# Kernel tuning notes

Hardware: AMD Instinct MI355X
Metric: run time of the kernel (lower is better)

Reference implementation:

```python
import jax, jax.numpy as jnp
import numpy as np

HIDDEN = 3072
HEADS = 32
HEAD_DIM = HIDDEN // HEADS  # 96


def setup_inputs() -> dict:
    key = jax.random.key(0)
    k1, k2, k3, k4 = jax.random.split(key, 4)
    B, S = 2, 2048
    x = jax.random.normal(k1, (B, S, HIDDEN), dtype=jnp.float32)
    # qkv_proj: Linear(hidden, 3*hidden, bias=False); torch weight is [out,in]
    w_qkv = jax.random.normal(k2, (3 * HIDDEN, HIDDEN), dtype=jnp.float32) * (HIDDEN ** -0.5)
    # o_proj: Linear(hidden, hidden) with bias
    w_o = jax.random.normal(k3, (HIDDEN, HIDDEN), dtype=jnp.float32) * (HIDDEN ** -0.5)
    b_o = jax.random.normal(k4, (HIDDEN,), dtype=jnp.float32) * 0.01
    return {"x": x, "w_qkv": w_qkv, "w_o": w_o, "b_o": b_o}


def reference(x, w_qkv, w_o, b_o):
    B, S, _ = x.shape
    qkv = jnp.einsum('bsh,oh->bso', x, w_qkv)  # [B,S,3*HIDDEN]
    q, k, v = jnp.split(qkv, 3, axis=-1)
    # [B,S,HIDDEN] -> [B,H,S,D]
    def split_heads(t):
        return t.reshape(B, S, HEADS, HEAD_DIM).transpose(0, 2, 1, 3)
    q, k, v = split_heads(q), split_heads(k), split_heads(v)
    scores = jnp.einsum('bhqd,bhkd->bhqk', q, k) / jnp.sqrt(jnp.float32(HEAD_DIM))
    attn = jax.nn.softmax(scores, axis=-1)
    out = jnp.einsum('bhqk,bhkd->bhqd', attn, v)  # [B,H,S,D]
    out = out.transpose(0, 2, 1, 3).reshape(B, S, HIDDEN)
    return jnp.einsum('bsh,oh->bso', out, w_o) + b_o
```

## Files before the change

### kernel.cpp

```cpp
#include <hip/hip_runtime.h>
#include <math.h>


typedef unsigned int u32;
typedef unsigned short u16;
typedef __attribute__((ext_vector_type(8))) short bf16x8;
typedef __attribute__((ext_vector_type(4))) float f32x4;
typedef __attribute__((ext_vector_type(16))) float f32x16;

#define MFMA(a, b, c) __builtin_amdgcn_mfma_f32_16x16x32_bf16((a), (b), (c), 0, 0, 0)
#define MFMA32(a, b, c) __builtin_amdgcn_mfma_f32_32x32x16_bf16((a), (b), (c), 0, 0, 0)

#define GLDS16(g, l) __builtin_amdgcn_global_load_lds( \
    (const __attribute__((address_space(1))) u32*)(g), \
    (__attribute__((address_space(3))) u32*)(l), 16, 0, 0)

__device__ __forceinline__ u16 f2bf(float f) {
  u32 u = __builtin_bit_cast(u32, f);
  return (u16)((u + 0x7fffu + ((u >> 16) & 1u)) >> 16);
}
__device__ __forceinline__ float bf2f(u16 h) {
  u32 u = ((u32)h) << 16;
  return __builtin_bit_cast(float, u);
}
__device__ __forceinline__ void split2(float f, u16& h, u16& l) {
  h = f2bf(f);
  l = f2bf(f - bf2f(h));
}
__device__ __forceinline__ bf16x8 ld16(const u16* p) {
  return *reinterpret_cast<const bf16x8*>(p);
}

__global__ void split_kernel(const float* __restrict__ src, u16* __restrict__ dst,
                             long n) {
  long i = ((long)blockIdx.x * 256 + threadIdx.x) * 4;
  if (i >= n) return;
  const float4 v = *reinterpret_cast<const float4*>(src + i);
  const u32 i32 = (u32)i;
  const u32 row = i32 / 3072u;
  const u32 col = i32 - row * 3072u;
  const long base = (long)row * 6144 + (col >> 5) * 64 + (col & 31);
  ushort4 h, l;
  split2(v.x, h.x, l.x);
  split2(v.y, h.y, l.y);
  split2(v.z, h.z, l.z);
  split2(v.w, h.w, l.w);
  *reinterpret_cast<ushort4*>(dst + base) = h;
  *reinterpret_cast<ushort4*>(dst + base + 32) = l;
}

template <int MODE>
__global__ __launch_bounds__(256, 2) void gemm32(
    const u16* __restrict__ A2, const u16* __restrict__ B2,
    int M, int N,
    u16* __restrict__ C2, float* __restrict__ Cf, const float* __restrict__ bias) {
  constexpr int NT = 96;
  __shared__ u16 ldsA[2][128 * 64];
  __shared__ u16 ldsB[2][192 * 64];
  const int tid = threadIdx.x;
  const int lane = tid & 63;
  const int w = tid >> 6;
  const int wm = w >> 1, wn = w & 1;
  const int l31 = lane & 31;
  const int l5 = lane >> 5;

  const int mt = M >> 7;
  const int nwg = gridDim.x;
  const int bid = blockIdx.x;
  const int wg = (bid & 7) * (nwg >> 3) + (bid >> 3);
  const int bm = wg % mt, bn = wg / mt;

  const int srow = lane >> 3;
  const int sgc = ((lane & 7) ^ srow ^ w) * 8;

  auto stA = [&](int buf, int kt, int j) {
    const int r = j * 32 + w * 8 + srow;
    GLDS16(A2 + (long)(bm * 128 + r) * 6144 + kt * 64 + sgc,
           &ldsA[buf][(j * 32 + w * 8) * 64]);
  };
  auto stB = [&](int buf, int kt, int j) {
    const int r = j * 32 + w * 8 + srow;
    GLDS16(B2 + (long)(bn * 192 + r) * 6144 + kt * 64 + sgc,
           &ldsB[buf][(j * 32 + w * 8) * 64]);
  };

  f32x16 acc[2][3];
#pragma unroll
  for (int m = 0; m < 2; ++m)
#pragma unroll
    for (int n = 0; n < 3; ++n)
#pragma unroll
      for (int j = 0; j < 16; ++j) acc[m][n][j] = 0.f;

  stA(0, 0, 0); stA(0, 0, 1); stA(0, 0, 2); stA(0, 0, 3);
  stB(0, 0, 0); stB(0, 0, 1); stB(0, 0, 2);
  stB(0, 0, 3); stB(0, 0, 4); stB(0, 0, 5);
  __syncthreads();

  const int aRow0 = wm * 64 + l31;
  const int bRow0 = wn * 96 + l31;
  const int rk = (lane & 7) ^ ((lane >> 3) & 3);

#define CSLOT(KS, PL) ((((KS)*2 + l5 + (PL)*4) ^ rk) * 8)
#define RD_PH(KS)                                                          \
  _Pragma("unroll") for (int n = 0; n < 3; ++n) {                          \
    const int off = (bRow0 + n * 32) * 64;                                 \
    b[n][0] = ld16(&LB[off + CSLOT(KS, 0)]);                               \
    b[n][1] = ld16(&LB[off + CSLOT(KS, 1)]);                               \
  }                                                                        \
  _Pragma("unroll") for (int m = 0; m < 2; ++m) {                          \
    const int off = (aRow0 + m * 32) * 64;                                 \
    a[m][0] = ld16(&LA[off + CSLOT(KS, 0)]);                               \
    a[m][1] = ld16(&LA[off + CSLOT(KS, 1)]);                               \
  }
#define DO_MFMA3()                                                         \
  __builtin_amdgcn_s_setprio(1);                                           \
  _Pragma("unroll") for (int m = 0; m < 2; ++m)                            \
  _Pragma("unroll") for (int n = 0; n < 3; ++n) {                          \
    acc[m][n] = MFMA32(a[m][0], b[n][0], acc[m][n]);                       \
    acc[m][n] = MFMA32(a[m][0], b[n][1], acc[m][n]);                       \
    acc[m][n] = MFMA32(a[m][1], b[n][0], acc[m][n]);                       \
  }                                                                        \
  __builtin_amdgcn_s_setprio(0);
#define PH_SYNC()                                                          \
  __builtin_amdgcn_s_barrier();                                            \
  asm volatile("s_waitcnt lgkmcnt(0)" ::: "memory");                       \
  __builtin_amdgcn_sched_barrier(0);

  for (int t = 0; t < NT; ++t) {
    const int cur = t & 1;
    const int nxt = cur ^ 1;
    const u16* LA = ldsA[cur];
    const u16* LB = ldsB[cur];
    bf16x8 a[2][2], b[3][2];
    RD_PH(0);
    if (t + 1 < NT) {
      stA(nxt, t + 1, 0); stA(nxt, t + 1, 1);
      stA(nxt, t + 1, 2); stA(nxt, t + 1, 3);
      stB(nxt, t + 1, 0); stB(nxt, t + 1, 1); stB(nxt, t + 1, 2);
      stB(nxt, t + 1, 3); stB(nxt, t + 1, 4); stB(nxt, t + 1, 5);
    }
    PH_SYNC();
    DO_MFMA3();
    __builtin_amdgcn_s_barrier();
    RD_PH(1);
    PH_SYNC();
    DO_MFMA3();
    asm volatile("s_waitcnt vmcnt(0)" ::: "memory");
    __builtin_amdgcn_s_barrier();
  }
#undef CSLOT
#undef RD_PH
#undef DO_MFMA3
#undef PH_SYNC

#pragma unroll
  for (int mf = 0; mf < 2; ++mf)
#pragma unroll
    for (int nf = 0; nf < 3; ++nf) {
      const int col = bn * 192 + wn * 96 + nf * 32 + l31;
#pragma unroll
      for (int reg = 0; reg < 16; ++reg) {
        const int rif = (reg & 3) + 8 * (reg >> 2) + 4 * l5;
        const long row = (long)bm * 128 + wm * 64 + mf * 32 + rif;
        const float v = acc[mf][nf][reg];
        if (MODE == 0) {
          const long idx = row * (2L * N) + (col >> 5) * 64 + (col & 31);
          u16 h, l;
          split2(v, h, l);
          C2[idx] = h;
          C2[idx + 32] = l;
        } else {
          Cf[row * N + col] = v + bias[col];
        }
      }
    }
}

__global__ void pack_k(const u16* __restrict__ QKV2, u16* __restrict__ Kp) {
  const int t = blockIdx.x * 256 + threadIdx.x;
  const int lane = t & 63;
  const int rec3 = t >> 6;
  const int c = rec3 % 3;
  const int kb = (rec3 / 3) & 127;
  const int hl = rec3 / 384;
  const int lr = lane & 15, lg = lane >> 4;
  const long src = ((long)((hl >> 5) * 2048 + kb * 16 + lr)) * 18432 +
                   (96 + (hl & 31) * 3 + c) * 64 + lg * 8;
  const long dst = ((long)rec3 * 2) * 512 + lane * 8;
  *reinterpret_cast<bf16x8*>(Kp + dst) = ld16(QKV2 + src);
  *reinterpret_cast<bf16x8*>(Kp + dst + 512) = ld16(QKV2 + src + 32);
}

__global__ __launch_bounds__(256) void pack_v(const u16* __restrict__ QKV2,
                                              u16* __restrict__ Vp) {
  __shared__ u16 sV[2][32 * 96];
  const int tid = threadIdx.x;
  const int hl = blockIdx.x >> 6;
  const int kq = blockIdx.x & 63;
  const long rowbase = ((long)((hl >> 5) * 2048 + kq * 32)) * 18432 +
                       (192 + (hl & 31) * 3) * 64;
#pragma unroll
  for (int i = 0; i < 3; ++i) {
    const int idx = i * 256 + tid;
    const int pl = idx / 384;
    const int r2 = idx % 384;
    const int row = r2 / 12, cu = r2 % 12;
    const long src = rowbase + (long)row * 18432 + (cu >> 2) * 64 + (cu & 3) * 8 + pl * 32;
    *reinterpret_cast<bf16x8*>(&sV[pl][row * 96 + cu * 8]) = ld16(QKV2 + src);
  }
  __syncthreads();
#pragma unroll
  for (int i = 0; i < 3; ++i) {
    const int idx = i * 256 + tid;
    const int lane = idx & 63;
    const int rl = idx >> 6;
    const int n = rl >> 1, pl = rl & 1;
    const int lr = lane & 15, lg = lane >> 4;
    bf16x8 o;
#pragma unroll
    for (int e = 0; e < 8; ++e) o[e] = (short)sV[pl][(lg * 8 + e) * 96 + n * 16 + lr];
    const long dst = ((((long)hl * 6 + n) * 64 + kq) * 2 + pl) * 512 + lane * 8;
    *reinterpret_cast<bf16x8*>(Vp + dst) = o;
  }
}

__global__ __launch_bounds__(256, 2) void attn_kernel(
    const u16* __restrict__ QKV2,
    const u16* __restrict__ Kp, const u16* __restrict__ Vp,
    u16* __restrict__ AO2) {
  __shared__ u16 kv[2][24 * 512];
  __shared__ u16 pb[4][2][2][512];
  const int lane = threadIdx.x & 63;
  const int wv = threadIdx.x >> 6;
  const int lr = lane & 15, lg = lane >> 4;

  const int nwg = gridDim.x;
  const int bid = blockIdx.x;
  const int wg = (bid & 7) * (nwg >> 3) + (bid >> 3);
  const int hl = wg >> 4;
  const int qblk = wg & 15;
  const int b = hl >> 5;
  const int q0 = qblk * 128 + wv * 32;

  bf16x8 qh[2][3], ql[2][3];
#pragma unroll
  for (int f = 0; f < 2; ++f) {
    const long qofs =
        ((long)(b * 2048 + q0 + f * 16 + lr)) * 18432 + ((hl & 31) * 3) * 64 + lg * 8;
#pragma unroll
    for (int c = 0; c < 3; ++c) {
      qh[f][c] = ld16(QKV2 + qofs + c * 64);
      ql[f][c] = ld16(QKV2 + qofs + c * 64 + 32);
    }
  }

  f32x4 o_acc[2][6];
#pragma unroll
  for (int f = 0; f < 2; ++f)
#pragma unroll
    for (int n = 0; n < 6; ++n)
#pragma unroll
      for (int j = 0; j < 4; ++j) o_acc[f][n][j] = 0.f;
  float lsum[2][4] = {{0.f, 0.f, 0.f, 0.f}, {0.f, 0.f, 0.f, 0.f}};

  const float scale = 0.10206207261596577f;

  auto stage = [&](int nb, int it) {
    const long kbase = ((long)hl * 768 + (long)it * 12) * 512;
    const long vbase = ((long)hl * 768 + (long)it * 2) * 512;
#pragma unroll
    for (int j = 0; j < 6; ++j) {
      const int r = wv * 6 + j;
      const u16* src;
      if (r < 12) {
        const int tt = r / 6, rc = r % 6;
        src = Kp + kbase + ((long)(tt * 6 + rc)) * 512 + lane * 8;
      } else {
        const int r2 = r - 12;
        src = Vp + vbase + ((long)((r2 >> 1) * 128 + (r2 & 1))) * 512 + lane * 8;
      }
      GLDS16(src, &kv[nb][r * 512]);
    }
  };

  stage(0, 0);
  __syncthreads();

  for (int it = 0; it < 64; ++it) {
    const int nb = it & 1;
    if (it < 63) stage(nb ^ 1, it + 1);
    const u16* L = kv[nb];

    bf16x8 kh0[3], kl0[3], kh1[3], kl1[3];
#pragma unroll
    for (int c = 0; c < 3; ++c) {
      kh0[c] = ld16(L + (c * 2 + 0) * 512 + lane * 8);
      kl0[c] = ld16(L + (c * 2 + 1) * 512 + lane * 8);
      kh1[c] = ld16(L + (6 + c * 2 + 0) * 512 + lane * 8);
      kl1[c] = ld16(L + (6 + c * 2 + 1) * 512 + lane * 8);
    }

    bf16x8 pah[2], pal[2];
#pragma unroll
    for (int f = 0; f < 2; ++f) {
      f32x4 s0, s1;
#pragma unroll
      for (int j = 0; j < 4; ++j) { s0[j] = 0.f; s1[j] = 0.f; }
#pragma unroll
      for (int c = 0; c < 3; ++c) {
        s0 = MFMA(qh[f][c], kh0[c], s0);
        s1 = MFMA(qh[f][c], kh1[c], s1);
        s0 = MFMA(qh[f][c], kl0[c], s0);
        s1 = MFMA(qh[f][c], kl1[c], s1);
        s0 = MFMA(ql[f][c], kh0[c], s0);
        s1 = MFMA(ql[f][c], kh1[c], s1);
      }
      u16* pbh = pb[wv][f][0];
      u16* pbl = pb[wv][f][1];
#pragma unroll
      for (int j = 0; j < 4; ++j) {
        const float p0 = __expf(fmaf(s0[j], scale, -12.f));
        const float p1 = __expf(fmaf(s1[j], scale, -12.f));
        lsum[f][j] += p0 + p1;
        const int r = lg * 4 + j;
        const int key = j ^ lg;
        u16 h, l;
        split2(p0, h, l);
        const int a0 = r * 32 + ((((lr >> 3) ^ key) & 3) << 3) + (lr & 7);
        pbh[a0] = h;
        pbl[a0] = l;
        split2(p1, h, l);
        const int a1 = r * 32 + ((((2 + (lr >> 3)) ^ key) & 3) << 3) + (lr & 7);
        pbh[a1] = h;
        pbl[a1] = l;
      }
      const int rkey = (lr & 3) ^ (lr >> 2);
      const int ra = lr * 32 + (((lg ^ rkey) & 3) << 3);
      pah[f] = ld16(&pbh[ra]);
      pal[f] = ld16(&pbl[ra]);
    }

#pragma unroll
    for (int n = 0; n < 6; ++n) {
      const bf16x8 vh = ld16(L + (12 + n * 2 + 0) * 512 + lane * 8);
      const bf16x8 vl = ld16(L + (12 + n * 2 + 1) * 512 + lane * 8);
#pragma unroll
      for (int f = 0; f < 2; ++f) {
        o_acc[f][n] = MFMA(pah[f], vh, o_acc[f][n]);
        o_acc[f][n] = MFMA(pah[f], vl, o_acc[f][n]);
        o_acc[f][n] = MFMA(pal[f], vh, o_acc[f][n]);
      }
    }
    __syncthreads();
  }

#pragma unroll
  for (int f = 0; f < 2; ++f) {
    float inv[4];
#pragma unroll
    for (int j = 0; j < 4; ++j) {
      float rs = lsum[f][j];
#pragma unroll
      for (int mk = 1; mk < 16; mk <<= 1) rs += __shfl_xor(rs, mk);
      inv[j] = 1.f / rs;
    }
#pragma unroll
    for (int n = 0; n < 6; ++n)
#pragma unroll
      for (int j = 0; j < 4; ++j) {
        const long row = (long)(b * 2048 + q0 + f * 16 + lg * 4 + j);
        const long idx =
            row * 6144 + ((hl & 31) * 3 + (n >> 1)) * 64 + (n & 1) * 16 + lr;
        u16 h, l;
        split2(o_acc[f][n][j] * inv[j], h, l);
        AO2[idx] = h;
        AO2[idx + 32] = l;
      }
  }
}

extern "C" void kernel_launch(void* const* d_in, const int* in_sizes, int n_in,
                              void* d_out, int out_size, void* d_ws, size_t ws_size,
                              hipStream_t stream) {
  const float* x = (const float*)d_in[0];
  const float* wqkv = (const float*)d_in[1];
  const float* wo = (const float*)d_in[2];
  const float* bo = (const float*)d_in[3];
  float* out = (float*)d_out;
  char* ws = (char*)d_ws;

  const size_t E_X = (size_t)4096 * 3072;
  const size_t E_WQ = (size_t)9216 * 3072;
  const size_t E_QKV = (size_t)4096 * 9216;
  const size_t E_WO = (size_t)3072 * 3072;

  u16* X2 = (u16*)ws;
  char* W0 = ws + 4 * E_X;
  u16* W2 = (u16*)W0;
  char* Q0 = W0 + 4 * E_WQ;
  u16* QKV2 = (u16*)Q0;
  char* V0 = Q0 + 4 * E_QKV;
  u16* VP = (u16*)V0;
  u16* KP = (u16*)ws;
  u16* AO2 = (u16*)W0;
  u16* WO2 = (u16*)(W0 + 4 * E_X);

  const size_t need = 4 * (E_X + E_WQ + E_QKV + E_X);
  if (ws_size < need) return;

  split_kernel<<<12288, 256, 0, stream>>>(x, X2, (long)E_X);
  split_kernel<<<27648, 256, 0, stream>>>(wqkv, W2, (long)E_WQ);
  gemm32<0><<<1536, 256, 0, stream>>>(X2, W2, 4096, 9216, QKV2, nullptr, nullptr);
  pack_k<<<6144, 256, 0, stream>>>(QKV2, KP);
  pack_v<<<4096, 256, 0, stream>>>(QKV2, VP);
  split_kernel<<<9216, 256, 0, stream>>>(wo, WO2, (long)E_WO);
  attn_kernel<<<1024, 256, 0, stream>>>(QKV2, KP, VP, AO2);
  gemm32<1><<<512, 256, 0, stream>>>(AO2, WO2, 4096, 3072, nullptr, out, bo);
}
```

Measured before the change: 1.216 ms.

## Fuse K/V packing into QKV GEMM epilogue via shared-memory transpose

The QKV projection GEMM now writes Q in split-bf16 layout directly. K and V tiles are staged through shared memory in the epilogue and written straight into the packed layouts the attention kernel consumes. This removes the separate pack_k and pack_v kernels and the full QKV intermediate round-trip through global memory, which also shrinks the workspace. In exchange the epilogue gains extra barriers and LDS traffic, including a strided per-element gather for V.

Result: faster. 1.160 ms (-4.6%).

```diff
diff --git a/kernel.cpp b/kernel.cpp
--- a/kernel.cpp
+++ b/kernel.cpp
@@ -52,11 +52,12 @@
 template <int MODE>
 __global__ __launch_bounds__(256, 2) void gemm32(
     const u16* __restrict__ A2, const u16* __restrict__ B2,
-    int M, int N,
-    u16* __restrict__ C2, float* __restrict__ Cf, const float* __restrict__ bias) {
+    int M, int N, u16* __restrict__ C2, u16* __restrict__ Kp,
+    u16* __restrict__ Vp, float* __restrict__ Cf, const float* __restrict__ bias) {
   constexpr int NT = 96;
-  __shared__ u16 ldsA[2][128 * 64];
-  __shared__ u16 ldsB[2][192 * 64];
+  __shared__ u16 shm[2 * 128 * 64 + 2 * 192 * 64];
+  u16* const uA = shm;
+  u16* const uB = shm + 2 * 128 * 64;
   const int tid = threadIdx.x;
   const int lane = tid & 63;
   const int w = tid >> 6;
@@ -76,12 +77,12 @@
   auto stA = [&](int buf, int kt, int j) {
     const int r = j * 32 + w * 8 + srow;
     GLDS16(A2 + (long)(bm * 128 + r) * 6144 + kt * 64 + sgc,
-           &ldsA[buf][(j * 32 + w * 8) * 64]);
+           &uA[buf * 8192 + (j * 32 + w * 8) * 64]);
   };
   auto stB = [&](int buf, int kt, int j) {
     const int r = j * 32 + w * 8 + srow;
     GLDS16(B2 + (long)(bn * 192 + r) * 6144 + kt * 64 + sgc,
-           &ldsB[buf][(j * 32 + w * 8) * 64]);
+           &uB[buf * 12288 + (j * 32 + w * 8) * 64]);
   };
 
   f32x16 acc[2][3];
@@ -130,8 +131,8 @@
   for (int t = 0; t < NT; ++t) {
     const int cur = t & 1;
     const int nxt = cur ^ 1;
-    const u16* LA = ldsA[cur];
-    const u16* LB = ldsB[cur];
+    const u16* LA = &uA[cur * 8192];
+    const u16* LB = &uB[cur * 12288];
     bf16x8 a[2][2], b[3][2];
     RD_PH(0);
     if (t + 1 < NT) {
@@ -154,79 +155,95 @@
 #undef DO_MFMA3
 #undef PH_SYNC
 
-#pragma unroll
-  for (int mf = 0; mf < 2; ++mf)
-#pragma unroll
-    for (int nf = 0; nf < 3; ++nf) {
-      const int col = bn * 192 + wn * 96 + nf * 32 + l31;
-#pragma unroll
-      for (int reg = 0; reg < 16; ++reg) {
-        const int rif = (reg & 3) + 8 * (reg >> 2) + 4 * l5;
-        const long row = (long)bm * 128 + wm * 64 + mf * 32 + rif;
-        const float v = acc[mf][nf][reg];
-        if (MODE == 0) {
-          const long idx = row * (2L * N) + (col >> 5) * 64 + (col & 31);
-          u16 h, l;
-          split2(v, h, l);
-          C2[idx] = h;
-          C2[idx + 32] = l;
-        } else {
-          Cf[row * N + col] = v + bias[col];
+  if (MODE == 1 || (MODE == 2 && bn < 16)) {
+#pragma unroll
+    for (int mf = 0; mf < 2; ++mf)
+#pragma unroll
+      for (int nf = 0; nf < 3; ++nf) {
+        const int col = bn * 192 + wn * 96 + nf * 32 + l31;
+#pragma unroll
+        for (int reg = 0; reg < 16; ++reg) {
+          const int rif = (reg & 3) + 8 * (reg >> 2) + 4 * l5;
+          const long row = (long)bm * 128 + wm * 64 + mf * 32 + rif;
+          const float v = acc[mf][nf][reg];
+          if (MODE == 1) {
+            Cf[row * N + col] = v + bias[col];
+          } else {
+            const long idx = row * 6144 + (col >> 5) * 64 + (col & 31);
+            u16 h, l;
+            split2(v, h, l);
+            C2[idx] = h;
+            C2[idx + 32] = l;
+          }
         }
       }
-    }
-}
-
-__global__ void pack_k(const u16* __restrict__ QKV2, u16* __restrict__ Kp) {
-  const int t = blockIdx.x * 256 + threadIdx.x;
-  const int lane = t & 63;
-  const int rec3 = t >> 6;
-  const int c = rec3 % 3;
-  const int kb = (rec3 / 3) & 127;
-  const int hl = rec3 / 384;
-  const int lr = lane & 15, lg = lane >> 4;
-  const long src = ((long)((hl >> 5) * 2048 + kb * 16 + lr)) * 18432 +
-                   (96 + (hl & 31) * 3 + c) * 64 + lg * 8;
-  const long dst = ((long)rec3 * 2) * 512 + lane * 8;
-  *reinterpret_cast<bf16x8*>(Kp + dst) = ld16(QKV2 + src);
-  *reinterpret_cast<bf16x8*>(Kp + dst + 512) = ld16(QKV2 + src + 32);
-}
-
-__global__ __launch_bounds__(256) void pack_v(const u16* __restrict__ QKV2,
-                                              u16* __restrict__ Vp) {
-  __shared__ u16 sV[2][32 * 96];
-  const int tid = threadIdx.x;
-  const int hl = blockIdx.x >> 6;
-  const int kq = blockIdx.x & 63;
-  const long rowbase = ((long)((hl >> 5) * 2048 + kq * 32)) * 18432 +
-                       (192 + (hl & 31) * 3) * 64;
-#pragma unroll
-  for (int i = 0; i < 3; ++i) {
-    const int idx = i * 256 + tid;
-    const int pl = idx / 384;
-    const int r2 = idx % 384;
-    const int row = r2 / 12, cu = r2 % 12;
-    const long src = rowbase + (long)row * 18432 + (cu >> 2) * 64 + (cu & 3) * 8 + pl * 32;
-    *reinterpret_cast<bf16x8*>(&sV[pl][row * 96 + cu * 8]) = ld16(QKV2 + src);
-  }
-  __syncthreads();
-#pragma unroll
-  for (int i = 0; i < 3; ++i) {
-    const int idx = i * 256 + tid;
-    const int lane = idx & 63;
-    const int rl = idx >> 6;
-    const int n = rl >> 1, pl = rl & 1;
-    const int lr = lane & 15, lg = lane >> 4;
-    bf16x8 o;
-#pragma unroll
-    for (int e = 0; e < 8; ++e) o[e] = (short)sV[pl][(lg * 8 + e) * 96 + n * 16 + lr];
-    const long dst = ((((long)hl * 6 + n) * 64 + kq) * 2 + pl) * 512 + lane * 8;
-    *reinterpret_cast<bf16x8*>(Vp + dst) = o;
+  } else if (MODE == 2) {
+    const bool isV = (bn >= 32);
+    const int hd0 = (bn - (isV ? 32 : 16)) * 2;
+    const int b = (bm * 128) >> 11;
+    const int s_loc = (bm * 128) & 2047;
+    u16* const P = shm;
+    u16* const dst = isV ? Vp : Kp;
+#pragma unroll
+    for (int hf = 0; hf < 2; ++hf) {
+      __syncthreads();
+      if (wm == hf) {
+#pragma unroll
+        for (int mf = 0; mf < 2; ++mf)
+#pragma unroll
+          for (int nf = 0; nf < 3; ++nf)
+#pragma unroll
+            for (int reg = 0; reg < 16; ++reg) {
+              const int rif = (reg & 3) + 8 * (reg >> 2) + 4 * l5;
+              const int row_l = mf * 32 + rif;
+              const int col_l = wn * 96 + nf * 32 + l31;
+              u16 h, l;
+              split2(acc[mf][nf][reg], h, l);
+              P[row_l * 200 + col_l] = h;
+              P[(64 + row_l) * 200 + col_l] = l;
+            }
+      }
+      __syncthreads();
+      const int lr = lane & 15, lg = lane >> 4;
+      if (!isV) {
+#pragma unroll
+        for (int i = 0; i < 12; ++i) {
+          const int ri = w * 12 + i;
+          const int pl = ri & 1;
+          const int kbi = (ri >> 1) & 3;
+          const int c = (ri >> 3) % 3;
+          const int hh = ri / 24;
+          const bf16x8 v =
+              ld16(&P[(pl * 64 + kbi * 16 + lr) * 200 + hh * 96 + c * 32 + lg * 8]);
+          const int hl = b * 32 + hd0 + hh;
+          const int kbg = ((s_loc + hf * 64) >> 4) + kbi;
+          const long rec3 = ((long)hl * 128 + kbg) * 3 + c;
+          *reinterpret_cast<bf16x8*>(dst + (rec3 * 2 + pl) * 512 + lane * 8) = v;
+        }
+      } else {
+#pragma unroll
+        for (int i = 0; i < 12; ++i) {
+          const int ri = w * 12 + i;
+          const int pl = ri & 1;
+          const int kq = (ri >> 1) & 1;
+          const int n = (ri >> 2) % 6;
+          const int hh = ri / 24;
+          bf16x8 v;
+#pragma unroll
+          for (int e = 0; e < 8; ++e)
+            v[e] = (short)P[(pl * 64 + kq * 32 + lg * 8 + e) * 200 + hh * 96 + n * 16 + lr];
+          const int hl = b * 32 + hd0 + hh;
+          const int kqg = ((s_loc + hf * 64) >> 5) + kq;
+          const long rec = (((long)hl * 6 + n) * 64 + kqg) * 2 + pl;
+          *reinterpret_cast<bf16x8*>(dst + rec * 512 + lane * 8) = v;
+        }
+      }
+    }
   }
 }
 
 __global__ __launch_bounds__(256, 2) void attn_kernel(
-    const u16* __restrict__ QKV2,
+    const u16* __restrict__ Q2,
     const u16* __restrict__ Kp, const u16* __restrict__ Vp,
     u16* __restrict__ AO2) {
   __shared__ u16 kv[2][24 * 512];
@@ -247,11 +264,11 @@
 #pragma unroll
   for (int f = 0; f < 2; ++f) {
     const long qofs =
-        ((long)(b * 2048 + q0 + f * 16 + lr)) * 18432 + ((hl & 31) * 3) * 64 + lg * 8;
+        ((long)(b * 2048 + q0 + f * 16 + lr)) * 6144 + ((hl & 31) * 3) * 64 + lg * 8;
 #pragma unroll
     for (int c = 0; c < 3; ++c) {
-      qh[f][c] = ld16(QKV2 + qofs + c * 64);
-      ql[f][c] = ld16(QKV2 + qofs + c * 64 + 32);
+      qh[f][c] = ld16(Q2 + qofs + c * 64);
+      ql[f][c] = ld16(Q2 + qofs + c * 64 + 32);
     }
   }
 
@@ -392,29 +409,26 @@
 
   const size_t E_X = (size_t)4096 * 3072;
   const size_t E_WQ = (size_t)9216 * 3072;
-  const size_t E_QKV = (size_t)4096 * 9216;
   const size_t E_WO = (size_t)3072 * 3072;
 
   u16* X2 = (u16*)ws;
   char* W0 = ws + 4 * E_X;
   u16* W2 = (u16*)W0;
-  char* Q0 = W0 + 4 * E_WQ;
-  u16* QKV2 = (u16*)Q0;
-  char* V0 = Q0 + 4 * E_QKV;
-  u16* VP = (u16*)V0;
-  u16* KP = (u16*)ws;
+  u16* Q2 = (u16*)(W0 + 4 * E_WQ);
+  u16* KP = Q2 + 2 * E_X;
+  u16* VP = KP + 2 * E_X;
   u16* AO2 = (u16*)W0;
   u16* WO2 = (u16*)(W0 + 4 * E_X);
 
-  const size_t need = 4 * (E_X + E_WQ + E_QKV + E_X);
+  const size_t need = 4 * (4 * E_X + E_WQ);
   if (ws_size < need) return;
 
   split_kernel<<<12288, 256, 0, stream>>>(x, X2, (long)E_X);
   split_kernel<<<27648, 256, 0, stream>>>(wqkv, W2, (long)E_WQ);
-  gemm32<0><<<1536, 256, 0, stream>>>(X2, W2, 4096, 9216, QKV2, nullptr, nullptr);
-  pack_k<<<6144, 256, 0, stream>>>(QKV2, KP);
-  pack_v<<<4096, 256, 0, stream>>>(QKV2, VP);
+  gemm32<2><<<1536, 256, 0, stream>>>(X2, W2, 4096, 9216, Q2, KP, VP,
+                                      nullptr, nullptr);
   split_kernel<<<9216, 256, 0, stream>>>(wo, WO2, (long)E_WO);
-  attn_kernel<<<1024, 256, 0, stream>>>(QKV2, KP, VP, AO2);
-  gemm32<1><<<512, 256, 0, stream>>>(AO2, WO2, 4096, 3072, nullptr, out, bo);
-}
+  attn_kernel<<<1024, 256, 0, stream>>>(Q2, KP, VP, AO2);
+  gemm32<1><<<512, 256, 0, stream>>>(AO2, WO2, 4096, 3072, nullptr, nullptr,
+                                     nullptr, out, bo);
+}
```
